# Kernel tuning notes

Measured on AMD Instinct MI355X. Metric: run time of the kernel, lower is better.

## Reference

```python
import jax, jax.numpy as jnp
import numpy as np

DIM = 1024
NUM_HEADS = 16
HEAD_DIM = DIM // NUM_HEADS
SCALE = HEAD_DIM ** -0.5
B, N = 2, 2048


def setup_inputs() -> dict:
    key = jax.random.key(0)
    k_x, k_qkv, k_prjw, k_prjb = jax.random.split(key, 4)
    # nn.Linear(dim, 3*dim, bias=False): weight [3*dim, dim]
    s = 1.0 / np.sqrt(DIM)
    return {
        "x": jax.random.normal(k_x, (B, N, DIM), dtype=jnp.float32),
        "w_qkv": jax.random.uniform(k_qkv, (3 * DIM, DIM), jnp.float32, -s, s),
        "w_prj": jax.random.uniform(k_prjw, (DIM, DIM), jnp.float32, -s, s),
        "b_prj": jax.random.uniform(k_prjb, (DIM,), jnp.float32, -s, s),
    }


def reference(x, w_qkv, w_prj, b_prj):
    Bb, Nn, C = x.shape
    qkv = jnp.einsum("bnc,dc->bnd", x, w_qkv)            # [B,N,3C]
    qkv = qkv.reshape(Bb, Nn, 3, NUM_HEADS, HEAD_DIM)
    qkv = jnp.transpose(qkv, (2, 0, 3, 1, 4))            # [3,B,H,N,hd]
    q, k, v = qkv[0], qkv[1], qkv[2]
    attn = jnp.einsum("bhqd,bhkd->bhqk", q, k) * SCALE   # [B,H,N,N]
    attn = jax.nn.softmax(attn, axis=-1)
    out = jnp.einsum("bhqk,bhkd->bhqd", attn, v)         # [B,H,N,hd]
    out = jnp.transpose(out, (0, 2, 1, 3)).reshape(Bb, Nn, C)
    # dropout layers are identity at eval / p=0
    return jnp.einsum("bnc,dc->bnd", out, w_prj) + b_prj
```

## Files before the change

kernel.cpp:

```cpp
#include <hip/hip_runtime.h>

typedef unsigned short u16;
typedef unsigned int u32;
typedef __attribute__((ext_vector_type(8))) short s16x8;
typedef __attribute__((ext_vector_type(4))) float f32x4;

#define DIM    1024
#define NHEADS 16
#define HD     64
#define NSEQ   2048
#define QKVN   3072

__device__ __forceinline__ u16 f2bf(float f) {
  u32 u = __float_as_uint(f);
  u += 0x7FFF + ((u >> 16) & 1);
  return (u16)(u >> 16);
}

__device__ __forceinline__ void async16(const u16* g, u16* l) {
  __builtin_amdgcn_global_load_lds(
      (const __attribute__((address_space(1))) unsigned int*)g,
      (__attribute__((address_space(3))) unsigned int*)l, 16, 0, 0);
}

__global__ void cast_all(const float* __restrict__ x, const float* __restrict__ wq,
                         const float* __restrict__ wp, u16* __restrict__ xo,
                         u16* __restrict__ wqo, u16* __restrict__ wpo) {
  int i = blockIdx.x * 256 + threadIdx.x;
  const float4* src; u16* dst; int off;
  if (i < 1048576)      { src = (const float4*)x;  dst = xo;  off = i; }
  else if (i < 1835008) { src = (const float4*)wq; dst = wqo; off = i - 1048576; }
  else                  { src = (const float4*)wp; dst = wpo; off = i - 1835008; }
  float4 f = src[off];
  ushort4 o;
  o.x = f2bf(f.x); o.y = f2bf(f.y); o.z = f2bf(f.z); o.w = f2bf(f.w);
  ((ushort4*)dst)[off] = o;
}

template <bool FINAL>
__global__ __launch_bounds__(256, 3) void gemm_bt(
    const u16* __restrict__ A, const u16* __restrict__ Bw, u16* __restrict__ qkv,
    u16* __restrict__ vt, const float* __restrict__ bias, float* __restrict__ outp) {
  constexpr int K = 1024;
  constexpr int BM = FINAL ? 64 : 128;
  constexpr int MT = FINAL ? 64 : 32;
  constexpr int IT = FINAL ? 2 : 4;
  constexpr int ACALLS = BM / 8;
  constexpr int TCALLS = ACALLS + 16;
  constexpr int PW = TCALLS / 4;
  const int bm = blockIdx.x % MT;
  const int bn = blockIdx.x / MT;
  const int tid = threadIdx.x;
  const int wave = tid >> 6, lane = tid & 63;
  const int q4 = lane >> 4, l15 = lane & 15;
  const int wm = wave >> 1, wn = wave & 1;
  const int m0 = bm * BM, n0 = bn * 128;

  __shared__ alignas(16) u16 lsA[BM * 64];
  __shared__ alignas(16) u16 lsB[128 * 64];

  f32x4 acc[IT][4];
#pragma unroll
  for (int i = 0; i < IT; i++)
#pragma unroll
    for (int j = 0; j < 4; j++) acc[i][j] = (f32x4){0.f, 0.f, 0.f, 0.f};

  for (int k0 = 0; k0 < K; k0 += 64) {
    __syncthreads();
#pragma unroll
    for (int j = 0; j < PW; ++j) {
      int t = wave * PW + j;
      if (t < ACALLS) {
        int lin = t * 64 + lane;
        int r = lin >> 3, cs = lin & 7, c = cs ^ (r & 7);
        async16(A + (size_t)(m0 + r) * K + k0 + c * 8, lsA + t * 512);
      } else {
        int tb = t - ACALLS;
        int lin = tb * 64 + lane;
        int r = lin >> 3, cs = lin & 7, c = cs ^ (r & 7);
        async16(Bw + (size_t)(n0 + r) * K + k0 + c * 8, lsB + tb * 512);
      }
    }
    __syncthreads();
#pragma unroll
    for (int kc = 0; kc < 2; ++kc) {
      s16x8 af[IT], bfr[4];
#pragma unroll
      for (int i = 0; i < IT; ++i) {
        int r = wm * (IT * 16) + i * 16 + l15;
        int c = (kc * 4 + q4) ^ (r & 7);
        af[i] = *(const s16x8*)(lsA + r * 64 + c * 8);
      }
#pragma unroll
      for (int j = 0; j < 4; ++j) {
        int r = wn * 64 + j * 16 + l15;
        int c = (kc * 4 + q4) ^ (r & 7);
        bfr[j] = *(const s16x8*)(lsB + r * 64 + c * 8);
      }
#pragma unroll
      for (int i = 0; i < IT; ++i)
#pragma unroll
        for (int j = 0; j < 4; ++j)
          acc[i][j] = __builtin_amdgcn_mfma_f32_16x16x32_bf16(af[i], bfr[j], acc[i][j], 0, 0, 0);
    }
  }

#pragma unroll
  for (int i = 0; i < IT; i++) {
#pragma unroll
    for (int j = 0; j < 4; j++) {
      int n = n0 + wn * 64 + j * 16 + l15;
      int mb = m0 + wm * (IT * 16) + i * 16 + q4 * 4;
      if (FINAL) {
#pragma unroll
        for (int r = 0; r < 4; r++)
          outp[(size_t)(mb + r) * DIM + n] = acc[i][j][r] + bias[n];
      } else if (n < 2048) {
#pragma unroll
        for (int r = 0; r < 4; r++)
          qkv[(size_t)(mb + r) * QKVN + n] = f2bf(acc[i][j][r]);
      } else {
        int b = mb >> 11, tok = mb & 2047;
        int h = (n >> 6) & 15, hd = n & 63;
        ushort4 pk;
        pk.x = f2bf(acc[i][j][0]); pk.y = f2bf(acc[i][j][1]);
        pk.z = f2bf(acc[i][j][2]); pk.w = f2bf(acc[i][j][3]);
        *(ushort4*)(vt + ((size_t)((b * NHEADS + h) * HD + hd)) * NSEQ + tok) = pk;
      }
    }
  }
}

__global__ __launch_bounds__(512, 4) void attn_kernel(const u16* __restrict__ qkv,
                                                      const u16* __restrict__ vt,
                                                      u16* __restrict__ aout) {
  const int blk = blockIdx.x;
  const int bh = blk >> 4, qt = blk & 15;
  const int b = bh >> 4, h = bh & 15;
  const int tid = threadIdx.x;
  const int wave = tid >> 6, lane = tid & 63;
  const int q4 = lane >> 4, l15 = lane & 15;

  __shared__ alignas(16) u16 lsK[128 * 64];
  __shared__ alignas(16) u16 lsV[64 * 128];
  __shared__ alignas(16) u16 lsP[8][16 * 72];

  const float QSCALE = 0.18033688011112042f;
  s16x8 aq[2];
#pragma unroll
  for (int kc = 0; kc < 2; ++kc) {
    int row = b * NSEQ + qt * 128 + wave * 16 + l15;
    uint4 d = *(const uint4*)(qkv + (size_t)row * QKVN + h * HD + kc * 32 + q4 * 8);
    u32 w[4] = {d.x, d.y, d.z, d.w};
    s16x8 f;
#pragma unroll
    for (int j = 0; j < 8; ++j) {
      u16 u = (u16)(w[j >> 1] >> ((j & 1) * 16));
      float v = __uint_as_float(((u32)u) << 16) * QSCALE;
      f[j] = (short)f2bf(v);
    }
    aq[kc] = f;
  }

  f32x4 o[4];
  float lsum[4] = {0.f, 0.f, 0.f, 0.f};
#pragma unroll
  for (int ht = 0; ht < 4; ++ht) o[ht] = (f32x4){0.f, 0.f, 0.f, 0.f};

  for (int kt = 0; kt < 16; ++kt) {
    __syncthreads();
#pragma unroll
    for (int j = 0; j < 2; ++j) {
      int t = wave * 2 + j;
      int lin = t * 64 + lane;
      int rK = lin >> 3, cK = (lin & 7) ^ (rK & 7);
      async16(qkv + (size_t)(b * NSEQ + kt * 128 + rK) * QKVN + DIM + h * HD + cK * 8,
              lsK + t * 512);
      int rV = lin >> 4, cV = (lin & 15) ^ (rV & 15);
      async16(vt + (size_t)(bh * HD + rV) * NSEQ + kt * 128 + cV * 8,
              lsV + t * 512);
    }
    __syncthreads();

#pragma unroll
    for (int half = 0; half < 2; ++half) {
      f32x4 s[4];
#pragma unroll
      for (int ct = 0; ct < 4; ++ct) s[ct] = (f32x4){0.f, 0.f, 0.f, 0.f};
#pragma unroll
      for (int kc = 0; kc < 2; ++kc) {
#pragma unroll
        for (int ct = 0; ct < 4; ++ct) {
          int r = half * 64 + ct * 16 + l15;
          int c = (kc * 4 + q4) ^ (r & 7);
          s16x8 bk = *(const s16x8*)(lsK + r * 64 + c * 8);
          s[ct] = __builtin_amdgcn_mfma_f32_16x16x32_bf16(aq[kc], bk, s[ct], 0, 0, 0);
        }
      }

#pragma unroll
      for (int ct = 0; ct < 4; ++ct)
#pragma unroll
        for (int r = 0; r < 4; ++r) {
          u32 u = __float_as_uint(exp2f(s[ct][r]));
          lsum[r] += __uint_as_float(u & 0xffff0000u);
          lsP[wave][(q4 * 4 + r) * 72 + ct * 16 + l15] = (u16)(u >> 16);
        }

#pragma unroll
      for (int kc = 0; kc < 2; ++kc) {
        s16x8 pa = *(const s16x8*)(lsP[wave] + l15 * 72 + kc * 32 + q4 * 8);
#pragma unroll
        for (int ht = 0; ht < 4; ++ht) {
          int r = ht * 16 + l15;
          int c = (half * 8 + kc * 4 + q4) ^ (r & 15);
          s16x8 vb = *(const s16x8*)(lsV + r * 128 + c * 8);
          o[ht] = __builtin_amdgcn_mfma_f32_16x16x32_bf16(pa, vb, o[ht], 0, 0, 0);
        }
      }
    }
  }

#pragma unroll
  for (int off = 1; off < 16; off <<= 1)
#pragma unroll
    for (int r = 0; r < 4; ++r) lsum[r] += __shfl_xor(lsum[r], off, 64);
  float inv[4];
#pragma unroll
  for (int r = 0; r < 4; ++r) inv[r] = 1.0f / lsum[r];

#pragma unroll
  for (int ht = 0; ht < 4; ++ht)
#pragma unroll
    for (int r = 0; r < 4; ++r) {
      int n = qt * 128 + wave * 16 + q4 * 4 + r;
      int col = h * HD + ht * 16 + l15;
      aout[(size_t)(b * NSEQ + n) * DIM + col] = f2bf(o[ht][r] * inv[r]);
    }
}

extern "C" void kernel_launch(void* const* d_in, const int* in_sizes, int n_in,
                              void* d_out, int out_size, void* d_ws, size_t ws_size,
                              hipStream_t stream) {
  const float* x     = (const float*)d_in[0];
  const float* w_qkv = (const float*)d_in[1];
  const float* w_prj = (const float*)d_in[2];
  const float* b_prj = (const float*)d_in[3];
  float* out = (float*)d_out;

  char* ws = (char*)d_ws;
  u16* x_bf    = (u16*)(ws);
  u16* wqkv_bf = (u16*)(ws + (size_t)(8u << 20));
  u16* wprj_bf = (u16*)(ws + (size_t)(14u << 20));
  u16* qkv     = (u16*)(ws + (size_t)(16u << 20));
  u16* vt      = (u16*)(ws + (size_t)(40u << 20));
  u16* aout    = (u16*)(ws + (size_t)(48u << 20));

  cast_all<<<8192, 256, 0, stream>>>(x, w_qkv, w_prj, x_bf, wqkv_bf, wprj_bf);
  gemm_bt<false><<<32 * 24, 256, 0, stream>>>(x_bf, wqkv_bf, qkv, vt, nullptr, nullptr);
  attn_kernel<<<512, 512, 0, stream>>>(qkv, vt, aout);
  gemm_bt<true><<<64 * 8, 256, 0, stream>>>(aout, wprj_bf, nullptr, nullptr, b_prj, out);
}
```

Measured before the change: 191.9 us.

## Split QKV GEMM, swap MFMA operands for row-contiguous vector stores, raw v_exp

The QKV projection is split into two launches: one for Q/K, which swaps MFMA operands so each lane holds 4 consecutive columns and writes ushort4 rows, and one for V with 64-row tiles that keeps the transposed vt store. The output projection also swaps operands, so it can do float4 bias loads and float4 stores instead of scalar strided stores. exp2f in attention is replaced by inline v_exp_f32 assembly to drop range-handling code. The split adds an extra launch and a smaller-tile V GEMM with less reuse. The raw exp instruction may handle denormal and extreme inputs differently from exp2f.

```diff
diff --git a/kernel.cpp b/kernel.cpp
--- a/kernel.cpp
+++ b/kernel.cpp
@@ -15,6 +15,12 @@
   u32 u = __float_as_uint(f);
   u += 0x7FFF + ((u >> 16) & 1);
   return (u16)(u >> 16);
+}
+
+__device__ __forceinline__ float vexp2(float x) {
+  float r;
+  asm volatile("v_exp_f32 %0, %1" : "=v"(r) : "v"(x));
+  return r;
 }
 
 __device__ __forceinline__ void async16(const u16* g, u16* l) {
@@ -37,24 +43,26 @@
   ((ushort4*)dst)[off] = o;
 }
 
-template <bool FINAL>
+template <int MODE>
 __global__ __launch_bounds__(256, 3) void gemm_bt(
     const u16* __restrict__ A, const u16* __restrict__ Bw, u16* __restrict__ qkv,
     u16* __restrict__ vt, const float* __restrict__ bias, float* __restrict__ outp) {
   constexpr int K = 1024;
-  constexpr int BM = FINAL ? 64 : 128;
-  constexpr int MT = FINAL ? 64 : 32;
-  constexpr int IT = FINAL ? 2 : 4;
+  constexpr int BM = (MODE == 0) ? 128 : 64;
+  constexpr int MT = (MODE == 0) ? 32 : 64;
+  constexpr int IT = (MODE == 0) ? 4 : 2;
   constexpr int ACALLS = BM / 8;
   constexpr int TCALLS = ACALLS + 16;
   constexpr int PW = TCALLS / 4;
+  constexpr bool TRANS = (MODE != 1);
   const int bm = blockIdx.x % MT;
   const int bn = blockIdx.x / MT;
   const int tid = threadIdx.x;
   const int wave = tid >> 6, lane = tid & 63;
   const int q4 = lane >> 4, l15 = lane & 15;
   const int wm = wave >> 1, wn = wave & 1;
-  const int m0 = bm * BM, n0 = bn * 128;
+  const int m0 = bm * BM;
+  const int n0 = (MODE == 1 ? 2048 : 0) + bn * 128;
 
   __shared__ alignas(16) u16 lsA[BM * 64];
   __shared__ alignas(16) u16 lsB[128 * 64];
@@ -100,8 +108,12 @@
 #pragma unroll
       for (int i = 0; i < IT; ++i)
 #pragma unroll
-        for (int j = 0; j < 4; ++j)
-          acc[i][j] = __builtin_amdgcn_mfma_f32_16x16x32_bf16(af[i], bfr[j], acc[i][j], 0, 0, 0);
+        for (int j = 0; j < 4; ++j) {
+          if (TRANS)
+            acc[i][j] = __builtin_amdgcn_mfma_f32_16x16x32_bf16(bfr[j], af[i], acc[i][j], 0, 0, 0);
+          else
+            acc[i][j] = __builtin_amdgcn_mfma_f32_16x16x32_bf16(af[i], bfr[j], acc[i][j], 0, 0, 0);
+        }
     }
   }
 
@@ -109,17 +121,23 @@
   for (int i = 0; i < IT; i++) {
 #pragma unroll
     for (int j = 0; j < 4; j++) {
-      int n = n0 + wn * 64 + j * 16 + l15;
-      int mb = m0 + wm * (IT * 16) + i * 16 + q4 * 4;
-      if (FINAL) {
-#pragma unroll
-        for (int r = 0; r < 4; r++)
-          outp[(size_t)(mb + r) * DIM + n] = acc[i][j][r] + bias[n];
-      } else if (n < 2048) {
-#pragma unroll
-        for (int r = 0; r < 4; r++)
-          qkv[(size_t)(mb + r) * QKVN + n] = f2bf(acc[i][j][r]);
+      if (MODE == 2) {
+        int m = m0 + wm * (IT * 16) + i * 16 + l15;
+        int nb = n0 + wn * 64 + j * 16 + q4 * 4;
+        float4 bv = *(const float4*)(bias + nb);
+        float4 v = {acc[i][j][0] + bv.x, acc[i][j][1] + bv.y,
+                    acc[i][j][2] + bv.z, acc[i][j][3] + bv.w};
+        *(float4*)(outp + (size_t)m * DIM + nb) = v;
+      } else if (MODE == 0) {
+        int m = m0 + wm * (IT * 16) + i * 16 + l15;
+        int nb = n0 + wn * 64 + j * 16 + q4 * 4;
+        ushort4 pk;
+        pk.x = f2bf(acc[i][j][0]); pk.y = f2bf(acc[i][j][1]);
+        pk.z = f2bf(acc[i][j][2]); pk.w = f2bf(acc[i][j][3]);
+        *(ushort4*)(qkv + (size_t)m * QKVN + nb) = pk;
       } else {
+        int n = n0 + wn * 64 + j * 16 + l15;
+        int mb = m0 + wm * (IT * 16) + i * 16 + q4 * 4;
         int b = mb >> 11, tok = mb & 2047;
         int h = (n >> 6) & 15, hd = n & 63;
         ushort4 pk;
@@ -202,7 +220,7 @@
       for (int ct = 0; ct < 4; ++ct)
 #pragma unroll
         for (int r = 0; r < 4; ++r) {
-          u32 u = __float_as_uint(exp2f(s[ct][r]));
+          u32 u = __float_as_uint(vexp2(s[ct][r]));
           lsum[r] += __uint_as_float(u & 0xffff0000u);
           lsP[wave][(q4 * 4 + r) * 72 + ct * 16 + l15] = (u16)(u >> 16);
         }
@@ -257,7 +275,8 @@
   u16* aout    = (u16*)(ws + (size_t)(48u << 20));
 
   cast_all<<<8192, 256, 0, stream>>>(x, w_qkv, w_prj, x_bf, wqkv_bf, wprj_bf);
-  gemm_bt<false><<<32 * 24, 256, 0, stream>>>(x_bf, wqkv_bf, qkv, vt, nullptr, nullptr);
+  gemm_bt<0><<<32 * 16, 256, 0, stream>>>(x_bf, wqkv_bf, qkv, vt, nullptr, nullptr);
+  gemm_bt<1><<<64 * 8, 256, 0, stream>>>(x_bf, wqkv_bf, qkv, vt, nullptr, nullptr);
   attn_kernel<<<512, 512, 0, stream>>>(qkv, vt, aout);
-  gemm_bt<true><<<64 * 8, 256, 0, stream>>>(aout, wprj_bf, nullptr, nullptr, b_prj, out);
-}
+  gemm_bt<2><<<64 * 8, 256, 0, stream>>>(aout, wprj_bf, nullptr, nullptr, b_prj, out);
+}
```

Measured after the change: 193.8 us. About the same (+1.0%).
